# Kernel tuning notes

Measured on AMD Instinct MI355X. Metric: run time of the kernel, lower is better.

## Reference

```python
import jax, jax.numpy as jnp
import numpy as np
import math

B, L, D, H = 2, 2048, 1024, 16
DH = D // H  # d_head = 64
FACTOR = 5


def setup_inputs() -> dict:
    key = jax.random.key(0)
    ks = jax.random.split(key, 6)
    s = 0.02
    x = jax.random.normal(ks[0], (B, L, D), jnp.float32)
    Wq = jax.random.normal(ks[1], (D, D), jnp.float32) * s
    bq = jnp.zeros((D,), jnp.float32)
    Wkv = jax.random.normal(ks[2], (2 * D, D), jnp.float32) * s
    bkv = jnp.zeros((2 * D,), jnp.float32)
    Wout = jax.random.normal(ks[3], (D, D), jnp.float32) * s
    bout = jnp.zeros((D,), jnp.float32)
    U = min(FACTOR * math.ceil(math.log(L)), L)  # 40
    index_sample = jax.random.randint(ks[4], (L, U), 0, L, dtype=jnp.int32)
    return {"x": x, "Wq": Wq, "bq": bq, "Wkv": Wkv, "bkv": bkv,
            "Wout": Wout, "bout": bout, "index_sample": index_sample,
            "factor": FACTOR}


def reference(x, Wq, bq, Wkv, bkv, Wout, bout, index_sample, factor):
    b, l, d = x.shape
    h, dh = H, DH
    scale = 1.0 / math.sqrt(dh)
    u = min(factor * math.ceil(math.log(l)), l)

    # projections (torch Linear: y = x @ W.T + b)
    Q = (x @ Wq.T + bq).reshape(b, l, h, dh).transpose(0, 2, 1, 3)   # [B,H,L,dh]
    KV = x @ Wkv.T + bkv
    K, V = jnp.split(KV, 2, axis=-1)
    K = K.reshape(b, l, h, dh).transpose(0, 2, 1, 3)                  # [B,H,L,dh]
    V = V.reshape(b, l, h, dh).transpose(0, 2, 1, 3)                  # [B,H,L,dh]

    # sampled QK: per query position l, dot with U sampled keys
    K_s = K[:, :, index_sample, :]                                    # [B,H,L,U,dh]
    QK = jnp.einsum('bhld,bhlud->bhlu', Q, K_s)                       # [B,H,L,U]
    M = QK.max(axis=-1) - QK.mean(axis=-1)                            # sparsity measure
    _, top_idx = jax.lax.top_k(M, u)                                  # [B,H,u]

    # full attention only for the top-u queries
    top_q = jnp.take_along_axis(Q, top_idx[..., None], axis=2)        # [B,H,u,dh]
    scores = jnp.einsum('bhud,bhkd->bhuk', top_q, K) * scale          # [B,H,u,L]
    attn = jax.nn.softmax(scores, axis=-1)
    ctx_update = jnp.einsum('bhuk,bhkd->bhud', attn, V)               # [B,H,u,dh]

    # mean-initialized context, scatter updates at top queries
    context = jnp.broadcast_to(V.mean(axis=2, keepdims=True), (b, h, l, dh))
    bI = jnp.arange(b)[:, None, None]
    hI = jnp.arange(h)[None, :, None]
    context = context.at[bI, hI, top_idx].set(ctx_update)             # [B,H,L,dh]

    context = context.transpose(0, 2, 1, 3).reshape(b, l, d)
    return context @ Wout.T + bout
```

## Files before the change

### kernel.cpp

```cpp
#include <hip/hip_runtime.h>
#include <math.h>

#define B_ 2
#define L_ 2048
#define D_ 1024
#define H_ 16
#define DH_ 64
#define U_ 40
#define SCALE_ 0.125f

typedef __attribute__((ext_vector_type(8))) short short8v;
typedef __attribute__((ext_vector_type(4))) float f32x4;
typedef __attribute__((ext_vector_type(4))) unsigned short ushort4v;

static __device__ __forceinline__ unsigned short bf16_rne(float f) {
  unsigned int u = __float_as_uint(f);
  u += 0x7fff + ((u >> 16) & 1);
  return (unsigned short)(u >> 16);
}
static __device__ __forceinline__ float bf16_f32(unsigned short h) {
  return __uint_as_float(((unsigned int)h) << 16);
}

static __device__ __forceinline__ void gload16(const unsigned short* src,
                                               unsigned short* lds) {
  __builtin_amdgcn_global_load_lds(
      (const __attribute__((address_space(1))) void*)src,
      (__attribute__((address_space(3))) void*)lds, 16, 0, 0);
}

__global__ __launch_bounds__(256) void split_all(
    const float* __restrict__ Wq, const float* __restrict__ Wkv,
    const float* __restrict__ X, unsigned short* __restrict__ Whi,
    unsigned short* __restrict__ Wlo, unsigned short* __restrict__ Xhi,
    unsigned short* __restrict__ Xlo, int nW) {
  int i = blockIdx.x * 256 + threadIdx.x;
  const int nq_q = (D_ * D_) / 4;
  float4 v;
  unsigned short *hi, *lo;
  int off;
  if (i < nW) {
    v = (i < nq_q) ? ((const float4*)Wq)[i] : ((const float4*)Wkv)[i - nq_q];
    hi = Whi; lo = Wlo; off = i;
  } else {
    off = i - nW;
    v = ((const float4*)X)[off];
    hi = Xhi; lo = Xlo;
  }
  float vv[4] = {v.x, v.y, v.z, v.w};
  ushort4v h, l;
#pragma unroll
  for (int e = 0; e < 4; ++e) {
    unsigned short hh = bf16_rne(vv[e]);
    h[e] = hh;
    l[e] = bf16_rne(vv[e] - bf16_f32(hh));
  }
  ((ushort4v*)hi)[off] = h;
  ((ushort4v*)lo)[off] = l;
}

template <bool XS>
__global__ __launch_bounds__(256) void gemm_qkv_mfma(
    const float* __restrict__ X,
    const unsigned short* __restrict__ Xhi,
    const unsigned short* __restrict__ Xlo,
    const unsigned short* __restrict__ Whi,
    const unsigned short* __restrict__ Wlo,
    const float* __restrict__ bq, const float* __restrict__ bkv,
    float* __restrict__ Qo, float* __restrict__ Ko, float* __restrict__ Vo) {
  __shared__ unsigned short Ah[128 * 32];
  __shared__ unsigned short Al[128 * 32];
  __shared__ unsigned short Bh[128 * 32];
  __shared__ unsigned short Bl[128 * 32];
  const int tid = threadIdx.x;
  const int lane = tid & 63;
  const int wave = tid >> 6;
  const int wm = wave >> 1, wn = wave & 1;
  const int row0 = blockIdx.y * 128;
  const int col0 = blockIdx.x * 128;

  f32x4 acc[4][4] = {};

  const int grow = lane >> 2;
  const int gg = lane & 3;

  for (int k0 = 0; k0 < D_; k0 += 32) {
#pragma unroll
    for (int j = 0; j < 2; ++j) {
      int c = wave + 4 * j;
      int row = c * 16 + grow;
      int gsrc = (gg ^ ((row >> 1) & 3)) << 3;
      size_t soffB = (size_t)(col0 + row) * D_ + k0 + gsrc;
      gload16(Whi + soffB, Bh + c * 512);
      gload16(Wlo + soffB, Bl + c * 512);
      if (XS) {
        size_t soffA = (size_t)(row0 + row) * D_ + k0 + gsrc;
        gload16(Xhi + soffA, Ah + c * 512);
        gload16(Xlo + soffA, Al + c * 512);
      }
    }
    if (!XS) {
#pragma unroll
      for (int rep = 0; rep < 2; ++rep) {
        int task = tid + rep * 256;
        int row = task >> 2;
        int gt = task & 3;
        const float* s = X + (size_t)(row0 + row) * D_ + k0 + gt * 8;
        float4 a0 = *(const float4*)s;
        float4 a1 = *(const float4*)(s + 4);
        float av[8] = {a0.x, a0.y, a0.z, a0.w, a1.x, a1.y, a1.z, a1.w};
        short8v hseg, lseg;
#pragma unroll
        for (int e = 0; e < 8; ++e) {
          unsigned short hh = bf16_rne(av[e]);
          hseg[e] = (short)hh;
          lseg[e] = (short)bf16_rne(av[e] - bf16_f32(hh));
        }
        int dst = row * 32 + ((gt ^ ((row >> 1) & 3)) << 3);
        *(short8v*)&Ah[dst] = hseg;
        *(short8v*)&Al[dst] = lseg;
      }
    }
    __syncthreads();

    short8v a_h[4], a_l[4], b_h[4], b_l[4];
    const int hs = lane >> 4;
#pragma unroll
    for (int mi = 0; mi < 4; ++mi) {
      int rr = wm * 64 + mi * 16 + (lane & 15);
      int off = rr * 32 + ((hs ^ ((rr >> 1) & 3)) << 3);
      a_h[mi] = *(const short8v*)&Ah[off];
      a_l[mi] = *(const short8v*)&Al[off];
    }
#pragma unroll
    for (int ni = 0; ni < 4; ++ni) {
      int rc = wn * 64 + ni * 16 + (lane & 15);
      int off = rc * 32 + ((hs ^ ((rc >> 1) & 3)) << 3);
      b_h[ni] = *(const short8v*)&Bh[off];
      b_l[ni] = *(const short8v*)&Bl[off];
    }
#pragma unroll
    for (int mi = 0; mi < 4; ++mi)
#pragma unroll
      for (int ni = 0; ni < 4; ++ni) {
        acc[mi][ni] = __builtin_amdgcn_mfma_f32_16x16x32_bf16(
            a_h[mi], b_h[ni], acc[mi][ni], 0, 0, 0);
        acc[mi][ni] = __builtin_amdgcn_mfma_f32_16x16x32_bf16(
            a_h[mi], b_l[ni], acc[mi][ni], 0, 0, 0);
        acc[mi][ni] = __builtin_amdgcn_mfma_f32_16x16x32_bf16(
            a_l[mi], b_h[ni], acc[mi][ni], 0, 0, 0);
      }
    __syncthreads();
  }

#pragma unroll
  for (int ni = 0; ni < 4; ++ni) {
    int c = col0 + wn * 64 + ni * 16 + (lane & 15);
    int which = c >> 10;
    int jj = c & (D_ - 1);
    int h = jj >> 6, dh = jj & 63;
    float bias = (c < D_) ? bq[c] : bkv[c - D_];
    float* dst = (which == 0) ? Qo : ((which == 1) ? Ko : Vo);
#pragma unroll
    for (int mi = 0; mi < 4; ++mi) {
#pragma unroll
      for (int reg = 0; reg < 4; ++reg) {
        int r = row0 + wm * 64 + mi * 16 + ((lane >> 4) << 2) + reg;
        int b = r >> 11, l = r & (L_ - 1);
        dst[(((size_t)b * H_ + h) * L_ + l) * DH_ + dh] =
            acc[mi][ni][reg] + bias;
      }
    }
  }
}

__global__ __launch_bounds__(256) void sample_m(
    const float* __restrict__ Q, const float* __restrict__ Kt,
    const int* __restrict__ idx, float* __restrict__ Mv) {
  int t = threadIdx.x;
  int w = t >> 6, lane = t & 63;
  int subl = lane >> 4, d16 = lane & 15;
  int gl = blockIdx.x * 16 + w * 4 + subl;
  int bh = gl >> 11, l = gl & (L_ - 1);
  const float4* Kb4 = (const float4*)(Kt + (size_t)bh * L_ * DH_);
  float4 q4 = ((const float4*)(Q + (size_t)gl * DH_))[d16];
  const int* irow = idx + l * U_;
  float mx = -INFINITY, sm = 0.f;
#pragma unroll 8
  for (int u = 0; u < U_; ++u) {
    int kl = irow[u];
    float4 k4 = Kb4[kl * 16 + d16];
    float p = q4.x * k4.x + q4.y * k4.y + q4.z * k4.z + q4.w * k4.w;
    p += __shfl_xor(p, 1);
    p += __shfl_xor(p, 2);
    p += __shfl_xor(p, 4);
    p += __shfl_xor(p, 8);
    mx = fmaxf(mx, p);
    sm += p;
  }
  if (d16 == 0) Mv[gl] = mx - sm * (1.0f / U_);
}

__global__ __launch_bounds__(64) void topk_kernel(
    const float* __restrict__ Mv, int* __restrict__ topIdx) {
  __shared__ float vals[L_];
  int lane = threadIdx.x;
  int bh = blockIdx.x;
  for (int j = 0; j < 32; ++j)
    vals[j * 64 + lane] = Mv[(size_t)bh * L_ + j * 64 + lane];
  __syncthreads();
  for (int it = 0; it < U_; ++it) {
    float bv = -INFINITY;
    int bi = 0x7fffffff;
    for (int j = 0; j < 32; ++j) {
      int i = j * 64 + lane;
      float v = vals[i];
      if (v > bv) { bv = v; bi = i; }
    }
#pragma unroll
    for (int off = 32; off > 0; off >>= 1) {
      float ov = __shfl_xor(bv, off);
      int oi = __shfl_xor(bi, off);
      if (ov > bv || (ov == bv && oi < bi)) { bv = ov; bi = oi; }
    }
    if (lane == 0) topIdx[bh * U_ + it] = bi;
    vals[bi] = -INFINITY;
    __syncthreads();
  }
}

__global__ __launch_bounds__(256) void attn_fused(
    const float* __restrict__ Q, const float* __restrict__ Kt,
    const float* __restrict__ Vt, const int* __restrict__ topIdx,
    float* __restrict__ ctxUpd, float* __restrict__ vmeanM) {
  int qc = blockIdx.x;
  int bh = blockIdx.y;
  __shared__ float Qs[5][DH_];
  __shared__ float Sv[5][L_];
  __shared__ float part[4][5][DH_];
  __shared__ float inv[5];
  __shared__ float vs[4][DH_];
  int t = threadIdx.x;
  int lane = t & 63, w = t >> 6;

  if (t < 80) {
    int q = t >> 4, c4 = t & 15;
    int ql = topIdx[bh * U_ + qc * 5 + q];
    *(float4*)&Qs[q][c4 * 4] =
        *(const float4*)&Q[((size_t)bh * L_ + ql) * DH_ + c4 * 4];
  }
  __syncthreads();

  const float* Kb = Kt + (size_t)bh * L_ * DH_;
  for (int kc = 0; kc < 8; ++kc) {
    int key = kc * 256 + t;
    const float* kr = Kb + (size_t)key * DH_;
    float acc[5];
#pragma unroll
    for (int q = 0; q < 5; ++q) acc[q] = 0.f;
#pragma unroll
    for (int i4 = 0; i4 < 16; ++i4) {
      float4 k4 = *(const float4*)(kr + i4 * 4);
#pragma unroll
      for (int q = 0; q < 5; ++q) {
        float4 qv = *(const float4*)&Qs[q][i4 * 4];
        acc[q] += k4.x * qv.x + k4.y * qv.y + k4.z * qv.z + k4.w * qv.w;
      }
    }
#pragma unroll
    for (int q = 0; q < 5; ++q) Sv[q][key] = acc[q] * SCALE_;
  }
  __syncthreads();

#pragma unroll
  for (int rep = 0; rep < 2; ++rep) {
    int r = (rep == 0) ? w : (w == 0 ? 4 : -1);
    if (r >= 0) {
      float mx = -INFINITY;
      for (int j = 0; j < 32; ++j) mx = fmaxf(mx, Sv[r][j * 64 + lane]);
#pragma unroll
      for (int off = 1; off < 64; off <<= 1)
        mx = fmaxf(mx, __shfl_xor(mx, off));
      float sm = 0.f;
      for (int j = 0; j < 32; ++j) {
        float e = __expf(Sv[r][j * 64 + lane] - mx);
        Sv[r][j * 64 + lane] = e;
        sm += e;
      }
#pragma unroll
      for (int off = 1; off < 64; off <<= 1) sm += __shfl_xor(sm, off);
      if (lane == 0) inv[r] = 1.0f / sm;
    }
  }
  __syncthreads();

  {
    const float* vb = Vt + ((size_t)bh * L_ + w * 512) * DH_ + lane;
    float acc[5];
#pragma unroll
    for (int q = 0; q < 5; ++q) acc[q] = 0.f;
    float vsum = 0.f;
    for (int k4 = 0; k4 < 128; ++k4) {
      float v0 = vb[(k4 * 4 + 0) * DH_];
      float v1 = vb[(k4 * 4 + 1) * DH_];
      float v2 = vb[(k4 * 4 + 2) * DH_];
      float v3 = vb[(k4 * 4 + 3) * DH_];
      vsum += (v0 + v1) + (v2 + v3);
      int k = w * 512 + k4 * 4;
#pragma unroll
      for (int q = 0; q < 5; ++q) {
        float4 p4 = *(const float4*)&Sv[q][k];
        acc[q] += p4.x * v0 + p4.y * v1 + p4.z * v2 + p4.w * v3;
      }
    }
#pragma unroll
    for (int q = 0; q < 5; ++q) part[w][q][lane] = acc[q];
    vs[w][lane] = vsum;
  }
  __syncthreads();

  for (int o = t; o < 5 * DH_; o += 256) {
    int q = o >> 6, dh = o & 63;
    float s = (part[0][q][dh] + part[1][q][dh]) +
              (part[2][q][dh] + part[3][q][dh]);
    ctxUpd[((size_t)bh * U_ + qc * 5 + q) * DH_ + dh] = s * inv[q];
  }
  if (qc == 0 && t < DH_)
    vmeanM[bh * DH_ + t] =
        ((vs[0][t] + vs[1][t]) + (vs[2][t] + vs[3][t])) * (1.0f / L_);
}

__global__ __launch_bounds__(256) void base_kernel(
    const float* __restrict__ vmeanM, const float* __restrict__ Wout,
    const float* __restrict__ bout, float* __restrict__ baseOut) {
  int bid = blockIdx.x;
  int b = bid >> 4, jc = bid & 15;
  int t = threadIdx.x;
  int j = jc * 64 + (t & 63);
  int isl = t >> 6;
  __shared__ float vm[D_];
  __shared__ float red[256];
  for (int i = t; i < D_; i += 256) vm[i] = vmeanM[b * D_ + i];
  __syncthreads();
  float s = 0.f;
  const float* wr = Wout + (size_t)j * D_ + isl * 256;
  const float* vv = vm + isl * 256;
  for (int i = 0; i < 256; i += 4) {
    float4 w = *(const float4*)(wr + i);
    s += vv[i] * w.x + vv[i + 1] * w.y + vv[i + 2] * w.z + vv[i + 3] * w.w;
  }
  red[t] = s; __syncthreads();
  if (isl == 0)
    baseOut[b * D_ + j] =
        red[t] + red[t + 64] + red[t + 128] + red[t + 192] + bout[j];
}

__global__ __launch_bounds__(256) void bcast_out(
    const float* __restrict__ baseIn, float* __restrict__ out) {
  size_t i4 = (size_t)blockIdx.x * 256 + threadIdx.x;
  size_t i = i4 * 4;
  int b = (int)(i >> 21);
  int col = (int)(i & (D_ - 1));
  *(float4*)(out + i) = *(const float4*)(baseIn + b * D_ + col);
}

__global__ __launch_bounds__(256) void corr_kernel(
    const int* __restrict__ topIdx, const float* __restrict__ ctxUpd,
    const float* __restrict__ vmeanM, const float* __restrict__ Wout,
    float* __restrict__ out) {
  int bhu = blockIdx.x;
  int bh = bhu / U_;
  int u = bhu - bh * U_;
  int h = bh & (H_ - 1), b = bh >> 4;
  int l = topIdx[bhu];
  __shared__ float dv[DH_];
  int t = threadIdx.x;
  if (t < DH_)
    dv[t] = ctxUpd[(size_t)bhu * DH_ + t] - vmeanM[bh * DH_ + t];
  __syncthreads();
  int sub = t & 3;
  int jbase = t >> 2;
  float* orow = out + ((size_t)b * L_ + l) * D_;
  const float* dvs = dv + sub * 16;
#pragma unroll
  for (int jc = 0; jc < 16; ++jc) {
    int j = jc * 64 + jbase;
    const float* wr = Wout + (size_t)j * D_ + h * DH_ + sub * 16;
    float s = 0.f;
#pragma unroll
    for (int i = 0; i < 16; i += 4) {
      float4 w = *(const float4*)(wr + i);
      s += dvs[i] * w.x + dvs[i + 1] * w.y + dvs[i + 2] * w.z +
           dvs[i + 3] * w.w;
    }
    s += __shfl_xor(s, 1);
    s += __shfl_xor(s, 2);
    if (sub == 0) atomicAdd(orow + j, s);
  }
}

extern "C" void kernel_launch(void* const* d_in, const int* in_sizes, int n_in,
                              void* d_out, int out_size, void* d_ws,
                              size_t ws_size, hipStream_t stream) {
  const float* x    = (const float*)d_in[0];
  const float* Wq   = (const float*)d_in[1];
  const float* bq   = (const float*)d_in[2];
  const float* Wkv  = (const float*)d_in[3];
  const float* bkv  = (const float*)d_in[4];
  const float* Wout = (const float*)d_in[5];
  const float* bout = (const float*)d_in[6];
  const int*   idx  = (const int*)d_in[7];
  float* out = (float*)d_out;

  float* ws = (float*)d_ws;
  const size_t NQ = (size_t)B_ * H_ * L_ * DH_;
  float* Q  = ws;
  float* Kt = Q + NQ;
  float* Vt = Kt + NQ;
  unsigned short* Whi = (unsigned short*)(Vt + NQ);
  unsigned short* Wlo = Whi + (size_t)3 * D_ * D_;
  unsigned short* Xhi = Wlo + (size_t)3 * D_ * D_;
  unsigned short* Xlo = Xhi + NQ;
  float* Mv     = Vt + NQ;
  float* ctxUpd = Mv + (size_t)B_ * H_ * L_;
  float* vmeanM = ctxUpd + (size_t)32 * U_ * DH_;
  float* baseB  = vmeanM + 32 * DH_;
  int*   topIdx = (int*)(baseB + B_ * D_);

  const bool xsplit = ws_size >= ((size_t)76 << 20);
  const int nW = 3 * D_ * D_ / 4;
  const int nX = (int)(NQ / 4);

  if (xsplit) {
    split_all<<<dim3((nW + nX) / 256), dim3(256), 0, stream>>>(
        Wq, Wkv, x, Whi, Wlo, Xhi, Xlo, nW);
    gemm_qkv_mfma<true>
        <<<dim3(3 * D_ / 128, B_ * L_ / 128), dim3(256), 0, stream>>>(
            x, Xhi, Xlo, Whi, Wlo, bq, bkv, Q, Kt, Vt);
  } else {
    split_all<<<dim3(nW / 256), dim3(256), 0, stream>>>(Wq, Wkv, x, Whi, Wlo,
                                                        Xhi, Xlo, nW);
    gemm_qkv_mfma<false>
        <<<dim3(3 * D_ / 128, B_ * L_ / 128), dim3(256), 0, stream>>>(
            x, Xhi, Xlo, Whi, Wlo, bq, bkv, Q, Kt, Vt);
  }
  sample_m<<<dim3(B_ * H_ * L_ / 16), dim3(256), 0, stream>>>(Q, Kt, idx, Mv);
  topk_kernel<<<dim3(B_ * H_), dim3(64), 0, stream>>>(Mv, topIdx);
  attn_fused<<<dim3(8, 32), dim3(256), 0, stream>>>(Q, Kt, Vt, topIdx, ctxUpd,
                                                    vmeanM);
  base_kernel<<<dim3(B_ * 16), dim3(256), 0, stream>>>(vmeanM, Wout, bout,
                                                       baseB);
  bcast_out<<<dim3(B_ * L_ * D_ / 1024), dim3(256), 0, stream>>>(baseB, out);
  corr_kernel<<<dim3(B_ * H_ * U_), dim3(256), 0, stream>>>(topIdx, ctxUpd,
                                                            vmeanM, Wout, out);
}
```

Before: 264.3 us.

## Fuse V-mean into QKV GEMM epilogue and merge attention with output correction

The V column sums are now computed in the QKV GEMM epilogue with atomics into a scratch buffer placed in the output tensor, which removes the V-sum loop from the attention kernel. The base/broadcast stage is moved before sampling, and the correction kernel is folded into the attention kernel, which processes 5 queries per Wout row load and drops the ctxUpd round trip and one launch. The cost is extra atomics in the GEMM epilogue, and the output buffer is reused as scratch before it is overwritten.

```diff
diff --git a/kernel.cpp b/kernel.cpp
--- a/kernel.cpp
+++ b/kernel.cpp
@@ -33,7 +33,10 @@
     const float* __restrict__ Wq, const float* __restrict__ Wkv,
     const float* __restrict__ X, unsigned short* __restrict__ Whi,
     unsigned short* __restrict__ Wlo, unsigned short* __restrict__ Xhi,
-    unsigned short* __restrict__ Xlo, int nW) {
+    unsigned short* __restrict__ Xlo, float* __restrict__ vmAcc, int nW) {
+  if (blockIdx.x == 0) {
+    for (int z = threadIdx.x; z < B_ * D_; z += 256) vmAcc[z] = 0.f;
+  }
   int i = blockIdx.x * 256 + threadIdx.x;
   const int nq_q = (D_ * D_) / 4;
   float4 v;
@@ -67,7 +70,8 @@
     const unsigned short* __restrict__ Whi,
     const unsigned short* __restrict__ Wlo,
     const float* __restrict__ bq, const float* __restrict__ bkv,
-    float* __restrict__ Qo, float* __restrict__ Ko, float* __restrict__ Vo) {
+    float* __restrict__ Qo, float* __restrict__ Ko, float* __restrict__ Vo,
+    float* __restrict__ vmAcc) {
   __shared__ unsigned short Ah[128 * 32];
   __shared__ unsigned short Al[128 * 32];
   __shared__ unsigned short Bh[128 * 32];
@@ -171,7 +175,55 @@
             acc[mi][ni][reg] + bias;
       }
     }
-  }
+    if (which == 2) {
+      float s = 0.f;
+#pragma unroll
+      for (int mi = 0; mi < 4; ++mi)
+#pragma unroll
+        for (int reg = 0; reg < 4; ++reg) s += acc[mi][ni][reg];
+      s += __shfl_xor(s, 16);
+      s += __shfl_xor(s, 32);
+      if ((lane >> 4) == 0)
+        atomicAdd(&vmAcc[(row0 >> 11) * D_ + jj], s + 64.0f * bias);
+    }
+  }
+}
+
+__global__ __launch_bounds__(256) void base_kernel(
+    const float* __restrict__ vmAcc, const float* __restrict__ Wout,
+    const float* __restrict__ bout, float* __restrict__ baseOut,
+    float* __restrict__ vmeanM) {
+  int bid = blockIdx.x;
+  int b = bid >> 4, jc = bid & 15;
+  int t = threadIdx.x;
+  int j = jc * 64 + (t & 63);
+  int isl = t >> 6;
+  __shared__ float vm[D_];
+  __shared__ float red[256];
+  for (int i = t; i < D_; i += 256) vm[i] = vmAcc[b * D_ + i] * (1.0f / L_);
+  __syncthreads();
+  if (jc == 0)
+    for (int i = t; i < D_; i += 256) vmeanM[b * D_ + i] = vm[i];
+  float s = 0.f;
+  const float* wr = Wout + (size_t)j * D_ + isl * 256;
+  const float* vv = vm + isl * 256;
+  for (int i = 0; i < 256; i += 4) {
+    float4 w = *(const float4*)(wr + i);
+    s += vv[i] * w.x + vv[i + 1] * w.y + vv[i + 2] * w.z + vv[i + 3] * w.w;
+  }
+  red[t] = s; __syncthreads();
+  if (isl == 0)
+    baseOut[b * D_ + j] =
+        red[t] + red[t + 64] + red[t + 128] + red[t + 192] + bout[j];
+}
+
+__global__ __launch_bounds__(256) void bcast_out(
+    const float* __restrict__ baseIn, float* __restrict__ out) {
+  size_t i4 = (size_t)blockIdx.x * 256 + threadIdx.x;
+  size_t i = i4 * 4;
+  int b = (int)(i >> 21);
+  int col = (int)(i & (D_ - 1));
+  *(float4*)(out + i) = *(const float4*)(baseIn + b * D_ + col);
 }
 
 __global__ __launch_bounds__(256) void sample_m(
@@ -229,17 +281,20 @@
   }
 }
 
-__global__ __launch_bounds__(256) void attn_fused(
+__global__ __launch_bounds__(256) void attn_corr(
     const float* __restrict__ Q, const float* __restrict__ Kt,
     const float* __restrict__ Vt, const int* __restrict__ topIdx,
-    float* __restrict__ ctxUpd, float* __restrict__ vmeanM) {
+    const float* __restrict__ vmeanM, const float* __restrict__ Wout,
+    float* __restrict__ out) {
   int qc = blockIdx.x;
   int bh = blockIdx.y;
+  int b = bh >> 4, h = bh & (H_ - 1);
   __shared__ float Qs[5][DH_];
   __shared__ float Sv[5][L_];
   __shared__ float part[4][5][DH_];
   __shared__ float inv[5];
-  __shared__ float vs[4][DH_];
+  __shared__ float dv[5][DH_];
+  __shared__ int lq[5];
   int t = threadIdx.x;
   int lane = t & 63, w = t >> 6;
 
@@ -249,6 +304,7 @@
     *(float4*)&Qs[q][c4 * 4] =
         *(const float4*)&Q[((size_t)bh * L_ + ql) * DH_ + c4 * 4];
   }
+  if (t < 5) lq[t] = topIdx[bh * U_ + qc * 5 + t];
   __syncthreads();
 
   const float* Kb = Kt + (size_t)bh * L_ * DH_;
@@ -299,13 +355,11 @@
     float acc[5];
 #pragma unroll
     for (int q = 0; q < 5; ++q) acc[q] = 0.f;
-    float vsum = 0.f;
     for (int k4 = 0; k4 < 128; ++k4) {
       float v0 = vb[(k4 * 4 + 0) * DH_];
       float v1 = vb[(k4 * 4 + 1) * DH_];
       float v2 = vb[(k4 * 4 + 2) * DH_];
       float v3 = vb[(k4 * 4 + 3) * DH_];
-      vsum += (v0 + v1) + (v2 + v3);
       int k = w * 512 + k4 * 4;
 #pragma unroll
       for (int q = 0; q < 5; ++q) {
@@ -315,7 +369,6 @@
     }
 #pragma unroll
     for (int q = 0; q < 5; ++q) part[w][q][lane] = acc[q];
-    vs[w][lane] = vsum;
   }
   __syncthreads();
 
@@ -323,79 +376,32 @@
     int q = o >> 6, dh = o & 63;
     float s = (part[0][q][dh] + part[1][q][dh]) +
               (part[2][q][dh] + part[3][q][dh]);
-    ctxUpd[((size_t)bh * U_ + qc * 5 + q) * DH_ + dh] = s * inv[q];
-  }
-  if (qc == 0 && t < DH_)
-    vmeanM[bh * DH_ + t] =
-        ((vs[0][t] + vs[1][t]) + (vs[2][t] + vs[3][t])) * (1.0f / L_);
-}
-
-__global__ __launch_bounds__(256) void base_kernel(
-    const float* __restrict__ vmeanM, const float* __restrict__ Wout,
-    const float* __restrict__ bout, float* __restrict__ baseOut) {
-  int bid = blockIdx.x;
-  int b = bid >> 4, jc = bid & 15;
-  int t = threadIdx.x;
-  int j = jc * 64 + (t & 63);
-  int isl = t >> 6;
-  __shared__ float vm[D_];
-  __shared__ float red[256];
-  for (int i = t; i < D_; i += 256) vm[i] = vmeanM[b * D_ + i];
-  __syncthreads();
-  float s = 0.f;
-  const float* wr = Wout + (size_t)j * D_ + isl * 256;
-  const float* vv = vm + isl * 256;
-  for (int i = 0; i < 256; i += 4) {
-    float4 w = *(const float4*)(wr + i);
-    s += vv[i] * w.x + vv[i + 1] * w.y + vv[i + 2] * w.z + vv[i + 3] * w.w;
-  }
-  red[t] = s; __syncthreads();
-  if (isl == 0)
-    baseOut[b * D_ + j] =
-        red[t] + red[t + 64] + red[t + 128] + red[t + 192] + bout[j];
-}
-
-__global__ __launch_bounds__(256) void bcast_out(
-    const float* __restrict__ baseIn, float* __restrict__ out) {
-  size_t i4 = (size_t)blockIdx.x * 256 + threadIdx.x;
-  size_t i = i4 * 4;
-  int b = (int)(i >> 21);
-  int col = (int)(i & (D_ - 1));
-  *(float4*)(out + i) = *(const float4*)(baseIn + b * D_ + col);
-}
-
-__global__ __launch_bounds__(256) void corr_kernel(
-    const int* __restrict__ topIdx, const float* __restrict__ ctxUpd,
-    const float* __restrict__ vmeanM, const float* __restrict__ Wout,
-    float* __restrict__ out) {
-  int bhu = blockIdx.x;
-  int bh = bhu / U_;
-  int u = bhu - bh * U_;
-  int h = bh & (H_ - 1), b = bh >> 4;
-  int l = topIdx[bhu];
-  __shared__ float dv[DH_];
-  int t = threadIdx.x;
-  if (t < DH_)
-    dv[t] = ctxUpd[(size_t)bhu * DH_ + t] - vmeanM[bh * DH_ + t];
-  __syncthreads();
+    dv[q][dh] = s * inv[q] - vmeanM[b * D_ + h * DH_ + dh];
+  }
+  __syncthreads();
+
   int sub = t & 3;
   int jbase = t >> 2;
-  float* orow = out + ((size_t)b * L_ + l) * D_;
-  const float* dvs = dv + sub * 16;
 #pragma unroll
   for (int jc = 0; jc < 16; ++jc) {
     int j = jc * 64 + jbase;
     const float* wr = Wout + (size_t)j * D_ + h * DH_ + sub * 16;
-    float s = 0.f;
-#pragma unroll
-    for (int i = 0; i < 16; i += 4) {
-      float4 w = *(const float4*)(wr + i);
-      s += dvs[i] * w.x + dvs[i + 1] * w.y + dvs[i + 2] * w.z +
-           dvs[i + 3] * w.w;
-    }
-    s += __shfl_xor(s, 1);
-    s += __shfl_xor(s, 2);
-    if (sub == 0) atomicAdd(orow + j, s);
+    float4 w0 = ((const float4*)wr)[0];
+    float4 w1 = ((const float4*)wr)[1];
+    float4 w2 = ((const float4*)wr)[2];
+    float4 w3 = ((const float4*)wr)[3];
+#pragma unroll
+    for (int q = 0; q < 5; ++q) {
+      const float* dq = &dv[q][sub * 16];
+      float s = dq[0] * w0.x + dq[1] * w0.y + dq[2] * w0.z + dq[3] * w0.w +
+                dq[4] * w1.x + dq[5] * w1.y + dq[6] * w1.z + dq[7] * w1.w +
+                dq[8] * w2.x + dq[9] * w2.y + dq[10] * w2.z + dq[11] * w2.w +
+                dq[12] * w3.x + dq[13] * w3.y + dq[14] * w3.z + dq[15] * w3.w;
+      s += __shfl_xor(s, 1);
+      s += __shfl_xor(s, 2);
+      if (sub == 0)
+        atomicAdd(out + ((size_t)b * L_ + lq[q]) * D_ + j, s);
+    }
   }
 }
 
@@ -422,10 +428,10 @@
   unsigned short* Xhi = Wlo + (size_t)3 * D_ * D_;
   unsigned short* Xlo = Xhi + NQ;
   float* Mv     = Vt + NQ;
-  float* ctxUpd = Mv + (size_t)B_ * H_ * L_;
-  float* vmeanM = ctxUpd + (size_t)32 * U_ * DH_;
-  float* baseB  = vmeanM + 32 * DH_;
+  float* vmeanM = Mv + (size_t)B_ * H_ * L_;
+  float* baseB  = vmeanM + B_ * D_;
   int*   topIdx = (int*)(baseB + B_ * D_);
+  float* vmAcc = out;
 
   const bool xsplit = ws_size >= ((size_t)76 << 20);
   const int nW = 3 * D_ * D_ / 4;
@@ -433,24 +439,22 @@
 
   if (xsplit) {
     split_all<<<dim3((nW + nX) / 256), dim3(256), 0, stream>>>(
-        Wq, Wkv, x, Whi, Wlo, Xhi, Xlo, nW);
+        Wq, Wkv, x, Whi, Wlo, Xhi, Xlo, vmAcc, nW);
     gemm_qkv_mfma<true>
         <<<dim3(3 * D_ / 128, B_ * L_ / 128), dim3(256), 0, stream>>>(
-            x, Xhi, Xlo, Whi, Wlo, bq, bkv, Q, Kt, Vt);
+            x, Xhi, Xlo, Whi, Wlo, bq, bkv, Q, Kt, Vt, vmAcc);
   } else {
     split_all<<<dim3(nW / 256), dim3(256), 0, stream>>>(Wq, Wkv, x, Whi, Wlo,
-                                                        Xhi, Xlo, nW);
+                                                        Xhi, Xlo, vmAcc, nW);
     gemm_qkv_mfma<false>
         <<<dim3(3 * D_ / 128, B_ * L_ / 128), dim3(256), 0, stream>>>(
-            x, Xhi, Xlo, Whi, Wlo, bq, bkv, Q, Kt, Vt);
-  }
+            x, Xhi, Xlo, Whi, Wlo, bq, bkv, Q, Kt, Vt, vmAcc);
+  }
+  base_kernel<<<dim3(B_ * 16), dim3(256), 0, stream>>>(vmAcc, Wout, bout,
+                                                       baseB, vmeanM);
+  bcast_out<<<dim3(B_ * L_ * D_ / 1024), dim3(256), 0, stream>>>(baseB, out);
   sample_m<<<dim3(B_ * H_ * L_ / 16), dim3(256), 0, stream>>>(Q, Kt, idx, Mv);
   topk_kernel<<<dim3(B_ * H_), dim3(64), 0, stream>>>(Mv, topIdx);
-  attn_fused<<<dim3(8, 32), dim3(256), 0, stream>>>(Q, Kt, Vt, topIdx, ctxUpd,
-                                                    vmeanM);
-  base_kernel<<<dim3(B_ * 16), dim3(256), 0, stream>>>(vmeanM, Wout, bout,
-                                                       baseB);
-  bcast_out<<<dim3(B_ * L_ * D_ / 1024), dim3(256), 0, stream>>>(baseB, out);
-  corr_kernel<<<dim3(B_ * H_ * U_), dim3(256), 0, stream>>>(topIdx, ctxUpd,
-                                                            vmeanM, Wout, out);
-}
+  attn_corr<<<dim3(8, 32), dim3(256), 0, stream>>>(Q, Kt, Vt, topIdx, vmeanM,
+                                                   Wout, out);
+}
```

After: 259.6 us. Within noise of the previous version (-1.8%).
